# Kernel tuning notes

Hardware: AMD Instinct MI355X
Metric: run time of the kernel (lower is better)

## Reference

```python
import jax, jax.numpy as jnp
import numpy as np

EPS = 1e-5

def layernorm(x, g, b):
    mu = jnp.mean(x, axis=-1, keepdims=True)
    var = jnp.mean((x - mu) ** 2, axis=-1, keepdims=True)
    return (x - mu) * jax.lax.rsqrt(var + EPS) * g + b

def setup_inputs() -> dict:
    key = jax.random.key(0)
    B, T, C, H = 4, 2048, 1024, 16
    hs = C // H  # 64
    ks = jax.random.split(key, 16)
    s_in = 1.0 / np.sqrt(C)
    s_hid = 1.0 / np.sqrt(4 * C)
    return {
        "x":   jax.random.normal(ks[0], (B, T, C), jnp.float32),
        # per-head projections, stacked over heads: [H, C, hs]
        "Wq":  jax.random.normal(ks[1], (H, C, hs), jnp.float32) * s_in,
        "Wk":  jax.random.normal(ks[2], (H, C, hs), jnp.float32) * s_in,
        "Wv":  jax.random.normal(ks[3], (H, C, hs), jnp.float32) * s_in,
        # output projection [C, C] (concat of heads -> C)
        "Wo":  jax.random.normal(ks[4], (C, C), jnp.float32) * s_in,
        "bo":  jnp.zeros((C,), jnp.float32),
        # layernorm params
        "g1":  jnp.ones((C,), jnp.float32),
        "be1": jnp.zeros((C,), jnp.float32),
        "g2":  jnp.ones((C,), jnp.float32),
        "be2": jnp.zeros((C,), jnp.float32),
        # feed-forward: C -> 4C -> C
        "W1":  jax.random.normal(ks[5], (C, 4 * C), jnp.float32) * s_in,
        "b1":  jnp.zeros((4 * C,), jnp.float32),
        "W2":  jax.random.normal(ks[6], (4 * C, C), jnp.float32) * s_hid,
        "b2":  jnp.zeros((C,), jnp.float32),
    }

def reference(x, Wq, Wk, Wv, Wo, bo, g1, be1, g2, be2, W1, b1, W2, b2):
    B, T, C = x.shape
    H, _, hs = Wq.shape
    scale = hs ** -0.5

    # --- self-attention on ln1(x) ---
    xn = layernorm(x, g1, be1)
    q = jnp.einsum('btc,hcd->bhtd', xn, Wq)
    k = jnp.einsum('btc,hcd->bhtd', xn, Wk)
    v = jnp.einsum('btc,hcd->bhtd', xn, Wv)
    scores = jnp.einsum('bhtd,bhsd->bhts', q, k) * scale  # [B,H,T,T]
    causal = jnp.tril(jnp.ones((T, T), dtype=bool))
    scores = jnp.where(causal, scores, jnp.finfo(scores.dtype).min)
    wei = jax.nn.softmax(scores, axis=-1)
    out = jnp.einsum('bhts,bhsd->bhtd', wei, v)           # [B,H,T,hs]
    out = out.transpose(0, 2, 1, 3).reshape(B, T, H * hs)  # concat heads
    x = x + out @ Wo + bo

    # --- feed-forward on ln2(x) ---
    xn2 = layernorm(x, g2, be2)
    h = jax.nn.relu(xn2 @ W1 + b1)
    x = x + h @ W2 + b2
    return x
```

## Files before the change

### kernel.cpp

```cpp
#include <hip/hip_runtime.h>
#include <hip/hip_bf16.h>

typedef __hip_bfloat16 bf16;
typedef __attribute__((ext_vector_type(8))) short bf16x8;
typedef __attribute__((ext_vector_type(4))) short s16x4;
typedef __attribute__((ext_vector_type(4))) float f32x4;
typedef __attribute__((ext_vector_type(2))) unsigned int u32x2;

__device__ __forceinline__ float b2f(bf16 v) { return __bfloat162float(v); }
__device__ __forceinline__ bf16  f2b(float v) { return __float2bfloat16(v); }
__device__ __forceinline__ float ldf(const bf16* p)  { return __bfloat162float(*p); }
__device__ __forceinline__ float ldf(const float* p) { return *p; }
__device__ __forceinline__ void  stf(bf16* p, float v)  { *p = __float2bfloat16(v); }
__device__ __forceinline__ void  stf(float* p, float v) { *p = v; }

__device__ __forceinline__ unsigned cvt_pk_bf16(float lo, float hi) {
    unsigned r;
    asm("v_cvt_pk_bf16_f32 %0, %1, %2" : "=v"(r) : "v"(lo), "v"(hi));
    return r;
}

__device__ __forceinline__ void ld4(const float* p, float* v) {
    float4 t = *(const float4*)p;
    v[0] = t.x; v[1] = t.y; v[2] = t.z; v[3] = t.w;
}
__device__ __forceinline__ void ld4(const bf16* p, float* v) {
    s16x4 t = *(const s16x4*)p;
#pragma unroll
    for (int j = 0; j < 4; ++j) { short s = t[j]; v[j] = b2f(*(bf16*)&s); }
}

__device__ __forceinline__ void load_lds16(const bf16* g, short* lds) {
    __builtin_amdgcn_global_load_lds(
        (const __attribute__((address_space(1))) unsigned int*)g,
        (__attribute__((address_space(3))) unsigned int*)lds, 16, 0, 0);
}

template<typename InT>
__global__ __launch_bounds__(256) void ln_kernel(const InT* __restrict__ x,
                                                 const float* __restrict__ g,
                                                 const float* __restrict__ b,
                                                 bf16* __restrict__ out)
{
    const int C = 1024;
    int row = blockIdx.x;
    int tid = threadIdx.x;
    const InT* xr = x + (size_t)row * C;

    float v[4];
    ld4(xr + tid * 4, v);
    float s = 0.f, s2 = 0.f;
#pragma unroll
    for (int i = 0; i < 4; ++i) { s += v[i]; s2 += v[i] * v[i]; }
#pragma unroll
    for (int off = 32; off > 0; off >>= 1) {
        s  += __shfl_down(s,  off, 64);
        s2 += __shfl_down(s2, off, 64);
    }
    __shared__ float red[8];
    int wave = tid >> 6;
    if ((tid & 63) == 0) { red[wave] = s; red[wave + 4] = s2; }
    __syncthreads();
    float ts  = red[0] + red[1] + red[2] + red[3];
    float ts2 = red[4] + red[5] + red[6] + red[7];
    float mu  = ts * (1.f / 1024.f);
    float var = ts2 * (1.f / 1024.f) - mu * mu;
    float rstd = rsqrtf(var + 1e-5f);

    float4 gg = *(const float4*)(g + tid * 4);
    float4 bb = *(const float4*)(b + tid * 4);
    float gj[4] = {gg.x, gg.y, gg.z, gg.w};
    float bj[4] = {bb.x, bb.y, bb.z, bb.w};
    s16x4 o4;
#pragma unroll
    for (int j = 0; j < 4; ++j) {
        bf16 ob = f2b((v[j] - mu) * rstd * gj[j] + bj[j]);
        o4[j] = *(short*)&ob;
    }
    *(s16x4*)(out + (size_t)row * C + tid * 4) = o4;
}

__global__ __launch_bounds__(256) void prep_weights(
    const float* __restrict__ Wq, const float* __restrict__ Wk,
    const float* __restrict__ Wv, const float* __restrict__ Wo,
    const float* __restrict__ W1, const float* __restrict__ W2,
    bf16* __restrict__ wqkvt, bf16* __restrict__ wot,
    bf16* __restrict__ w1t, bf16* __restrict__ w2t)
{
    __shared__ float t[32][33];
    int tx = threadIdx.x & 31, ty = threadIdx.x >> 5;
    int id = blockIdx.x;
    const float* in; bf16* out; int in_ld, out_ld, n0, k0;
    if (id < 3072) {
        const float* Ws[3] = {Wq, Wk, Wv};
        int m = id >> 10, r = id & 1023;
        int z = r >> 6, rt = r & 63;
        in = Ws[m] + z * 65536;
        out = wqkvt + (size_t)(m * 1024 + z * 64) * 1024;
        in_ld = 64; out_ld = 1024;
        n0 = (rt & 1) * 32; k0 = (rt >> 1) * 32;
    } else if (id < 4096) {
        int r = id - 3072;
        in = Wo; out = wot; in_ld = 1024; out_ld = 1024;
        n0 = (r & 31) * 32; k0 = (r >> 5) * 32;
    } else if (id < 8192) {
        int r = id - 4096;
        in = W1; out = w1t; in_ld = 4096; out_ld = 1024;
        n0 = (r & 127) * 32; k0 = (r >> 7) * 32;
    } else {
        int r = id - 8192;
        in = W2; out = w2t; in_ld = 1024; out_ld = 4096;
        n0 = (r & 31) * 32; k0 = (r >> 5) * 32;
    }
#pragma unroll
    for (int i = 0; i < 4; ++i)
        t[ty + i * 8][tx] = in[(size_t)(k0 + ty + i * 8) * in_ld + n0 + tx];
    __syncthreads();
#pragma unroll
    for (int i = 0; i < 4; ++i)
        out[(size_t)(n0 + ty + i * 8) * out_ld + k0 + tx] = f2b(t[tx][ty + i * 8]);
}

__global__ __launch_bounds__(256) void vt_kernel(
    const bf16* __restrict__ qkv, bf16* __restrict__ vt, int T)
{
    __shared__ float t[32][33];
    int tx = threadIdx.x & 31, ty = threadIdx.x >> 5;
    int z = blockIdx.z, b = z >> 4, h = z & 15;
    const bf16* in = qkv + (size_t)b * T * 3072 + 2048 + h * 64;
    bf16* out = vt + (size_t)z * 64 * T;
    int n0 = blockIdx.x * 32, k0 = blockIdx.y * 32;
#pragma unroll
    for (int i = 0; i < 4; ++i)
        t[ty + i * 8][tx] = b2f(in[(size_t)(k0 + ty + i * 8) * 3072 + n0 + tx]);
    __syncthreads();
#pragma unroll
    for (int i = 0; i < 4; ++i)
        out[(size_t)(n0 + ty + i * 8) * T + k0 + tx] = f2b(t[tx][ty + i * 8]);
}

template<bool RELU, bool HAS_BIAS, typename OutT>
__global__ __launch_bounds__(512, 2) void gemm8p(
    const bf16* __restrict__ A, int lda,
    const bf16* __restrict__ Bt, int ldb,
    const float* __restrict__ bias,
    OutT* __restrict__ Cm, int ldc,
    int M, int N, int K)
{
    __shared__ short As[4][8192];
    __shared__ short Bs[4][8192];
    int tid = threadIdx.x, wv = tid >> 6, ln = tid & 63;
    int quad = ln >> 4, lane15 = ln & 15;

    int nbn = N >> 8;
    int nwg = gridDim.x;
    int f2 = (blockIdx.x & 7) * (nwg >> 3) + (blockIdx.x >> 3);
    int by = f2 / nbn, bx = f2 % nbn;
    int bm0 = by << 8, bn0 = bx << 8;

    int wr = wv >> 2, wc = wv & 3;
    const int NT = K >> 5;

    int sr = tid >> 2;
    int sc = ((tid & 3) ^ ((sr >> 1) & 3)) * 8;
    const bf16* Ab1 = A  + (size_t)(bm0 + sr) * lda + sc;
    const bf16* Ab2 = A  + (size_t)(bm0 + 128 + sr) * lda + sc;
    const bf16* Bb1 = Bt + (size_t)(bn0 + sr) * ldb + sc;
    const bf16* Bb2 = Bt + (size_t)(bn0 + 128 + sr) * ldb + sc;

#define STAGE_A8(bf_, u_) { \
    load_lds16(Ab1 + (u_) * 32, &As[bf_][wv * 512]); \
    load_lds16(Ab2 + (u_) * 32, &As[bf_][4096 + wv * 512]); }
#define STAGE_B8(bf_, u_) { \
    load_lds16(Bb1 + (u_) * 32, &Bs[bf_][wv * 512]); \
    load_lds16(Bb2 + (u_) * 32, &Bs[bf_][4096 + wv * 512]); }

    f32x4 acc[8][4] = {};
    int arow = wr * 128 + lane15;
    int brow = wc * 64 + lane15;
    int sw = (quad ^ ((lane15 >> 1) & 3)) * 8;

    STAGE_A8(0, 0); STAGE_B8(0, 0);
    STAGE_A8(1, 1); STAGE_B8(1, 1);
    STAGE_A8(2, 2); STAGE_B8(2, 2);
    asm volatile("s_waitcnt vmcnt(8)" ::: "memory");
    __builtin_amdgcn_s_barrier();

    for (int t = 0; t < NT; ++t) {
        int buf = t & 3;
        const short* Al = &As[buf][0];
        const short* Bl = &Bs[buf][0];

        bf16x8 af[4], bfr[4];
#pragma unroll
        for (int mi = 0; mi < 4; ++mi)
            af[mi] = *(const bf16x8*)&Al[(arow + mi * 16) * 32 + sw];
#pragma unroll
        for (int ni = 0; ni < 4; ++ni)
            bfr[ni] = *(const bf16x8*)&Bl[(brow + ni * 16) * 32 + sw];
        if (t + 3 < NT) STAGE_A8((t + 3) & 3, t + 3);
        __builtin_amdgcn_s_barrier();
        __builtin_amdgcn_s_setprio(1);
#pragma unroll
        for (int mi = 0; mi < 4; ++mi)
#pragma unroll
            for (int ni = 0; ni < 4; ++ni)
                acc[mi][ni] = __builtin_amdgcn_mfma_f32_16x16x32_bf16(
                    af[mi], bfr[ni], acc[mi][ni], 0, 0, 0);
        __builtin_amdgcn_s_setprio(0);
        __builtin_amdgcn_s_barrier();

        bf16x8 ag[4];
#pragma unroll
        for (int mi = 0; mi < 4; ++mi)
            ag[mi] = *(const bf16x8*)&Al[(arow + (mi + 4) * 16) * 32 + sw];
        if (t + 3 < NT) STAGE_B8((t + 3) & 3, t + 3);
        if (t < NT - 3) {
            asm volatile("s_waitcnt vmcnt(8)" ::: "memory");
        } else if (t == NT - 3) {
            asm volatile("s_waitcnt vmcnt(4)" ::: "memory");
        } else if (t == NT - 2) {
            asm volatile("s_waitcnt vmcnt(0)" ::: "memory");
        }
        __builtin_amdgcn_s_barrier();
        __builtin_amdgcn_s_setprio(1);
#pragma unroll
        for (int mi = 0; mi < 4; ++mi)
#pragma unroll
            for (int ni = 0; ni < 4; ++ni)
                acc[mi + 4][ni] = __builtin_amdgcn_mfma_f32_16x16x32_bf16(
                    ag[mi], bfr[ni], acc[mi + 4][ni], 0, 0, 0);
        __builtin_amdgcn_s_setprio(0);
        __builtin_amdgcn_s_barrier();
    }

#undef STAGE_A8
#undef STAGE_B8

#pragma unroll
    for (int mi = 0; mi < 8; ++mi) {
#pragma unroll
        for (int r = 0; r < 4; ++r) {
            int gm = bm0 + wr * 128 + mi * 16 + quad * 4 + r;
#pragma unroll
            for (int ni = 0; ni < 4; ++ni) {
                int gn = bn0 + wc * 64 + ni * 16 + lane15;
                float v = acc[mi][ni][r];
                if (HAS_BIAS) v += bias[gn];
                if (RELU)     v = fmaxf(v, 0.f);
                stf(Cm + (size_t)gm * ldc + gn, v);
            }
        }
    }
}

template<int BK, bool RELU, bool HAS_BIAS, bool HAS_RES, typename ResT, typename OutT>
__global__ __launch_bounds__(256) void gemm_bt(
    const bf16* __restrict__ A, int lda,
    const bf16* __restrict__ Bt, int ldb,
    const float* __restrict__ bias,
    const ResT* __restrict__ res, int ldr,
    OutT* __restrict__ Cm, int ldc,
    int M, int N, int K)
{
    __shared__ short As[2][128 * BK];
    __shared__ short Bs[2][128 * BK];
    int tid = threadIdx.x, wv = tid >> 6, ln = tid & 63;

    int f = blockIdx.x + blockIdx.y * gridDim.x;
    int nby = gridDim.y;
    int by = f % nby, bx = f / nby;
    int bm0 = by * 128, bn0 = bx * 128;

    int wm = (wv & 1) * 64, wn = (wv >> 1) * 64;
    int quad = ln >> 4, lane15 = ln & 15;

    f32x4 acc[4][4] = {};

    const bf16* Ab = A + (size_t)bm0 * lda;
    const bf16* Bb = Bt + (size_t)bn0 * ldb;

    auto stage = [&](int buf, int kk) {
        if constexpr (BK == 32) {
            int srow = ln >> 2;
            int scol = (((ln & 3) ^ ((ln >> 3) & 3)) * 8);
#pragma unroll
            for (int i = 0; i < 2; ++i) {
                int ch = wv + i * 4;
                load_lds16(Ab + (size_t)(ch * 16 + srow) * lda + kk + scol,
                           &As[buf][ch * 16 * 32]);
                load_lds16(Bb + (size_t)(ch * 16 + srow) * ldb + kk + scol,
                           &Bs[buf][ch * 16 * 32]);
            }
        } else {
            int srow = ln >> 3;
            int scol = ((ln & 7) ^ srow) * 8;
#pragma unroll
            for (int i = 0; i < 4; ++i) {
                int r0 = i * 32 + wv * 8;
                load_lds16(Ab + (size_t)(r0 + srow) * lda + kk + scol,
                           &As[buf][r0 * 64]);
                load_lds16(Bb + (size_t)(r0 + srow) * ldb + kk + scol,
                           &Bs[buf][r0 * 64]);
            }
        }
    };

    stage(0, 0);
    __syncthreads();

    int cur = 0;
    for (int k0 = 0; k0 < K; k0 += BK) {
        if (k0 + BK < K) stage(cur ^ 1, k0 + BK);
        if constexpr (BK == 32) {
            int sw = (quad ^ ((lane15 >> 1) & 3)) * 8;
            bf16x8 af[4], bfr[4];
#pragma unroll
            for (int mi = 0; mi < 4; ++mi)
                af[mi] = *(const bf16x8*)&As[cur][(wm + mi * 16 + lane15) * 32 + sw];
#pragma unroll
            for (int ni = 0; ni < 4; ++ni)
                bfr[ni] = *(const bf16x8*)&Bs[cur][(wn + ni * 16 + lane15) * 32 + sw];
#pragma unroll
            for (int mi = 0; mi < 4; ++mi)
#pragma unroll
                for (int ni = 0; ni < 4; ++ni)
                    acc[mi][ni] = __builtin_amdgcn_mfma_f32_16x16x32_bf16(
                        af[mi], bfr[ni], acc[mi][ni], 0, 0, 0);
        } else {
#pragma unroll
            for (int ks = 0; ks < 2; ++ks) {
                int sw = (((ks * 4 + quad) ^ (lane15 & 7)) * 8);
                bf16x8 af[4], bfr[4];
#pragma unroll
                for (int mi = 0; mi < 4; ++mi)
                    af[mi] = *(const bf16x8*)&As[cur][(wm + mi * 16 + lane15) * 64 + sw];
#pragma unroll
                for (int ni = 0; ni < 4; ++ni)
                    bfr[ni] = *(const bf16x8*)&Bs[cur][(wn + ni * 16 + lane15) * 64 + sw];
#pragma unroll
                for (int mi = 0; mi < 4; ++mi)
#pragma unroll
                    for (int ni = 0; ni < 4; ++ni)
                        acc[mi][ni] = __builtin_amdgcn_mfma_f32_16x16x32_bf16(
                            af[mi], bfr[ni], acc[mi][ni], 0, 0, 0);
            }
        }
        __syncthreads();
        cur ^= 1;
    }

#pragma unroll
    for (int mi = 0; mi < 4; ++mi) {
#pragma unroll
        for (int r = 0; r < 4; ++r) {
            int gm = bm0 + wm + mi * 16 + quad * 4 + r;
#pragma unroll
            for (int ni = 0; ni < 4; ++ni) {
                int gn = bn0 + wn + ni * 16 + lane15;
                float v = acc[mi][ni][r];
                if (HAS_BIAS) v += bias[gn];
                if (HAS_RES)  v += ldf(res + (size_t)gm * ldr + gn);
                if (RELU)     v = fmaxf(v, 0.f);
                stf(Cm + (size_t)gm * ldc + gn, v);
            }
        }
    }
}

__device__ __forceinline__ void attn_tile_q(
    const short* __restrict__ Ks, const short* __restrict__ Vs,
    short* __restrict__ Psw,
    const bf16x8* qf, f32x4* oacc, float& lrun,
    int ktbase, int qmin, int quad, int lane15, int r7)
{
    const float scale2 = 0.18033688011112042f;
    const int PS = 72;
    f32x4 sacc[4] = {};
    __builtin_amdgcn_s_setprio(1);
#pragma unroll
    for (int ks = 0; ks < 2; ++ks) {
        int so = ((ks * 4 + quad) ^ r7) * 8;
#pragma unroll
        for (int mi = 0; mi < 4; ++mi) {
            bf16x8 kf = *(const bf16x8*)&Ks[(mi * 16 + lane15) * 64 + so];
            sacc[mi] = __builtin_amdgcn_mfma_f32_16x16x32_bf16(kf, qf[ks], sacc[mi], 0, 0, 0);
        }
    }
    __builtin_amdgcn_s_setprio(0);

    if (ktbase + 63 > qmin) {
        int ql = qmin + lane15;
#pragma unroll
        for (int mi = 0; mi < 4; ++mi)
#pragma unroll
            for (int r = 0; r < 4; ++r)
                if (ktbase + mi * 16 + quad * 4 + r > ql) sacc[mi][r] = -3e38f;
    }

    float psum = 0.f;
#pragma unroll
    for (int mi = 0; mi < 4; ++mi) {
        float p[4];
#pragma unroll
        for (int r = 0; r < 4; ++r) {
            p[r] = exp2f(sacc[mi][r] * scale2);
            psum += p[r];
        }
        u32x2 pu;
        pu[0] = cvt_pk_bf16(p[0], p[1]);
        pu[1] = cvt_pk_bf16(p[2], p[3]);
        *(u32x2*)&Psw[lane15 * PS + mi * 16 + quad * 4] = pu;
    }
    lrun += psum;

    __builtin_amdgcn_s_setprio(1);
#pragma unroll
    for (int ks = 0; ks < 2; ++ks) {
        int so = ((ks * 4 + quad) ^ r7) * 8;
        bf16x8 pf = *(const bf16x8*)&Psw[lane15 * PS + ks * 32 + quad * 8];
#pragma unroll
        for (int di = 0; di < 4; ++di) {
            bf16x8 vf = *(const bf16x8*)&Vs[(di * 16 + lane15) * 64 + so];
            oacc[di] = __builtin_amdgcn_mfma_f32_16x16x32_bf16(vf, pf, oacc[di], 0, 0, 0);
        }
    }
    __builtin_amdgcn_s_setprio(0);
}

__global__ __launch_bounds__(512, 4) void attn_kernel(
    const bf16* __restrict__ qkv, const bf16* __restrict__ vt,
    bf16* __restrict__ o, int T)
{
    const int LDQ = 3072;
    const int PS = 72;
    int bx = blockIdx.x;
    int qta = 15 - bx;
    int qtb = bx;
    int h = blockIdx.y, b = blockIdx.z;
    int tid = threadIdx.x, wv = tid >> 6, ln = tid & 63;
    int quad = ln >> 4, lane15 = ln & 15, r7 = lane15 & 7;

    __shared__ short KV[2][2][64 * 64];
    __shared__ short Ps[2][8][16 * PS];

    int lr = ln >> 3;
    int lc = ((ln & 7) ^ lr) * 8;

    const bf16* kbase = qkv + (size_t)(b * T) * LDQ + 1024 + h * 64;
    const bf16* vbase = vt + (size_t)((b * 16 + h) * 64) * T;

#pragma unroll
    for (int i = 0; i < 2; ++i) {
        int ch = wv * 2 + i;
        load_lds16(qkv + (size_t)(b * T + qta * 128 + ch * 8 + lr) * LDQ + h * 64 + lc,
                   &KV[0][0][ch * 512]);
        load_lds16(qkv + (size_t)(b * T + qtb * 128 + ch * 8 + lr) * LDQ + h * 64 + lc,
                   &KV[1][0][ch * 512]);
    }
    __syncthreads();
    bf16x8 qfa[2], qfb[2];
#pragma unroll
    for (int ks = 0; ks < 2; ++ks) {
        int off = (wv * 16 + lane15) * 64 + (((ks * 4 + quad) ^ r7) * 8);
        qfa[ks] = *(const bf16x8*)&KV[0][0][off];
        qfb[ks] = *(const bf16x8*)&KV[1][0][off];
    }
    __syncthreads();

    f32x4 oacca[4] = {}, oaccb[4] = {};
    float lra = 0.f, lrb = 0.f;
    int qmina = qta * 128 + wv * 16;
    int qminb = qtb * 128 + wv * 16;
    int ntiles = 2 * qta + 2;

    const bf16* kp = kbase + (size_t)(wv * 8 + lr) * LDQ + lc;
    const bf16* vp = vbase + (size_t)(wv * 8 + lr) * T + lc;
    load_lds16(kp, &KV[0][0][wv * 8 * 64]);
    load_lds16(vp, &KV[0][1][wv * 8 * 64]);

    for (int kt = 0; kt < ntiles; ++kt) {
        __syncthreads();
        if (kt + 1 < ntiles) {
            int nb = (kt + 1) & 1;
            kp += 64 * LDQ;
            vp += 64;
            load_lds16(kp, &KV[nb][0][wv * 8 * 64]);
            load_lds16(vp, &KV[nb][1][wv * 8 * 64]);
        }
        const short* Ks = &KV[kt & 1][0][0];
        const short* Vs = &KV[kt & 1][1][0];
        int kb = kt * 64;

        if (kb <= qmina + 15)
            attn_tile_q(Ks, Vs, &Ps[0][wv][0], qfa, oacca, lra,
                        kb, qmina, quad, lane15, r7);
        if (kb <= qminb + 15)
            attn_tile_q(Ks, Vs, &Ps[1][wv][0], qfb, oaccb, lrb,
                        kb, qminb, quad, lane15, r7);
    }

    lra += __shfl_xor(lra, 16, 64);
    lra += __shfl_xor(lra, 32, 64);
    float inva = 1.f / lra;
    size_t rowa = (size_t)(b * T + qta * 128 + wv * 16 + lane15);
#pragma unroll
    for (int di = 0; di < 4; ++di) {
        u32x2 ou;
        ou[0] = cvt_pk_bf16(oacca[di][0] * inva, oacca[di][1] * inva);
        ou[1] = cvt_pk_bf16(oacca[di][2] * inva, oacca[di][3] * inva);
        *(u32x2*)&o[rowa * 1024 + h * 64 + di * 16 + quad * 4] = ou;
    }

    lrb += __shfl_xor(lrb, 16, 64);
    lrb += __shfl_xor(lrb, 32, 64);
    float invb = 1.f / lrb;
    size_t rowb = (size_t)(b * T + qtb * 128 + wv * 16 + lane15);
#pragma unroll
    for (int di = 0; di < 4; ++di) {
        u32x2 ou;
        ou[0] = cvt_pk_bf16(oaccb[di][0] * invb, oaccb[di][1] * invb);
        ou[1] = cvt_pk_bf16(oaccb[di][2] * invb, oaccb[di][3] * invb);
        *(u32x2*)&o[rowb * 1024 + h * 64 + di * 16 + quad * 4] = ou;
    }
}

extern "C" void kernel_launch(void* const* d_in, const int* in_sizes, int n_in,
                              void* d_out, int out_size, void* d_ws, size_t ws_size,
                              hipStream_t stream)
{
    (void)in_sizes; (void)n_in; (void)out_size; (void)ws_size;
    const float* x   = (const float*)d_in[0];
    const float* Wq  = (const float*)d_in[1];
    const float* Wk  = (const float*)d_in[2];
    const float* Wv  = (const float*)d_in[3];
    const float* Wo  = (const float*)d_in[4];
    const float* bo  = (const float*)d_in[5];
    const float* g1  = (const float*)d_in[6];
    const float* be1 = (const float*)d_in[7];
    const float* g2  = (const float*)d_in[8];
    const float* be2 = (const float*)d_in[9];
    const float* W1  = (const float*)d_in[10];
    const float* b1  = (const float*)d_in[11];
    const float* W2  = (const float*)d_in[12];
    const float* b2  = (const float*)d_in[13];

    const int T = 2048, M = 4 * T;
    const size_t MB = 1ull << 20;
    char* ws = (char*)d_ws;

    bf16*  xn    = (bf16*)(ws + 0 * MB);
    bf16*  qkv   = (bf16*)(ws + 16 * MB);
    bf16*  vt    = (bf16*)(ws + 64 * MB);
    bf16*  wqkvt = (bf16*)(ws + 80 * MB);
    bf16*  x1b   = (bf16*)(ws + 80 * MB);
    bf16*  wot   = (bf16*)(ws + 96 * MB);
    bf16*  xn2   = (bf16*)(ws + 96 * MB);
    bf16*  w1t   = (bf16*)(ws + 112 * MB);
    bf16*  w2t   = (bf16*)(ws + 120 * MB);
    bf16*  attnb = (bf16*)(ws + 0 * MB);
    bf16*  hb    = (bf16*)(ws + 0 * MB);

    dim3 blk(256);

    prep_weights<<<12288, blk, 0, stream>>>(Wq, Wk, Wv, Wo, W1, W2,
                                            wqkvt, wot, w1t, w2t);

    ln_kernel<float><<<M, blk, 0, stream>>>(x, g1, be1, xn);

    gemm8p<false, false, bf16><<<dim3(384), dim3(512), 0, stream>>>(
        xn, 1024, wqkvt, 1024, nullptr, qkv, 3072, M, 3072, 1024);

    vt_kernel<<<dim3(2, T / 32, 64), blk, 0, stream>>>(qkv, vt, T);

    attn_kernel<<<dim3(8, 16, 4), dim3(512), 0, stream>>>(qkv, vt, attnb, T);

    gemm_bt<32, false, true, true, float, bf16><<<dim3(8, 64), blk, 0, stream>>>(
        attnb, 1024, wot, 1024, bo, x, 1024, x1b, 1024, M, 1024, 1024);

    ln_kernel<bf16><<<M, blk, 0, stream>>>(x1b, g2, be2, xn2);

    gemm8p<true, true, bf16><<<dim3(512), dim3(512), 0, stream>>>(
        xn2, 1024, w1t, 1024, b1, hb, 4096, M, 4096, 1024);

    gemm_bt<64, false, true, true, bf16, float><<<dim3(8, 64), blk, 0, stream>>>(
        hb, 4096, w2t, 4096, b2, x1b, 1024, (float*)d_out, 1024, M, 1024, 4096);
}
```

Measured before the change: 486.8 us.

## Switch attention to 32x32 MFMA tiles with register-resident softmax probabilities

Rewrites the attention inner tile to use 32x32x16 bf16 MFMAs with 256-row query tiles per block, so each wave handles 32 queries. The softmax probabilities stay in registers and are reshuffled with permlane32_swap instead of being staged through LDS. The dual-query path now shares each K/V fragment load across both query tiles. Q fragments are loaded directly from global memory rather than via LDS. The trade-off is higher register pressure: launch bounds drop to 2 blocks per SM and the grid is halved, which reduces occupancy and parallelism.

```diff
diff --git a/kernel.cpp b/kernel.cpp
--- a/kernel.cpp
+++ b/kernel.cpp
@@ -5,7 +5,9 @@
 typedef __attribute__((ext_vector_type(8))) short bf16x8;
 typedef __attribute__((ext_vector_type(4))) short s16x4;
 typedef __attribute__((ext_vector_type(4))) float f32x4;
+typedef __attribute__((ext_vector_type(16))) float f32x16;
 typedef __attribute__((ext_vector_type(2))) unsigned int u32x2;
+typedef __attribute__((ext_vector_type(4))) unsigned int u32x4;
 
 __device__ __forceinline__ float b2f(bf16 v) { return __bfloat162float(v); }
 __device__ __forceinline__ bf16  f2b(float v) { return __float2bfloat16(v); }
@@ -368,81 +370,106 @@
     }
 }
 
-__device__ __forceinline__ void attn_tile_q(
+template<bool DUAL>
+__device__ __forceinline__ void attn_tile32(
     const short* __restrict__ Ks, const short* __restrict__ Vs,
-    short* __restrict__ Psw,
-    const bf16x8* qf, f32x4* oacc, float& lrun,
-    int ktbase, int qmin, int quad, int lane15, int r7)
+    const bf16x8* qfa, const bf16x8* qfb,
+    f32x16* oa, f32x16* ob, float& lra, float& lrb,
+    int kb, int qmina, int qminb, int l31, int hi, int l7)
 {
     const float scale2 = 0.18033688011112042f;
-    const int PS = 72;
-    f32x4 sacc[4] = {};
+    f32x16 sa[2] = {};
+    f32x16 sb[2] = {};
+
     __builtin_amdgcn_s_setprio(1);
 #pragma unroll
-    for (int ks = 0; ks < 2; ++ks) {
-        int so = ((ks * 4 + quad) ^ r7) * 8;
-#pragma unroll
-        for (int mi = 0; mi < 4; ++mi) {
-            bf16x8 kf = *(const bf16x8*)&Ks[(mi * 16 + lane15) * 64 + so];
-            sacc[mi] = __builtin_amdgcn_mfma_f32_16x16x32_bf16(kf, qf[ks], sacc[mi], 0, 0, 0);
+    for (int ts = 0; ts < 2; ++ts) {
+#pragma unroll
+        for (int ks = 0; ks < 4; ++ks) {
+            bf16x8 kf = *(const bf16x8*)&Ks[(ts * 32 + l31) * 64 + (((ks * 2 + hi) ^ l7) * 8)];
+            sa[ts] = __builtin_amdgcn_mfma_f32_32x32x16_bf16(kf, qfa[ks], sa[ts], 0, 0, 0);
+            if (DUAL)
+                sb[ts] = __builtin_amdgcn_mfma_f32_32x32x16_bf16(kf, qfb[ks], sb[ts], 0, 0, 0);
         }
     }
     __builtin_amdgcn_s_setprio(0);
 
-    if (ktbase + 63 > qmin) {
-        int ql = qmin + lane15;
-#pragma unroll
-        for (int mi = 0; mi < 4; ++mi)
-#pragma unroll
-            for (int r = 0; r < 4; ++r)
-                if (ktbase + mi * 16 + quad * 4 + r > ql) sacc[mi][r] = -3e38f;
-    }
-
-    float psum = 0.f;
-#pragma unroll
-    for (int mi = 0; mi < 4; ++mi) {
-        float p[4];
-#pragma unroll
-        for (int r = 0; r < 4; ++r) {
-            p[r] = exp2f(sacc[mi][r] * scale2);
-            psum += p[r];
-        }
-        u32x2 pu;
-        pu[0] = cvt_pk_bf16(p[0], p[1]);
-        pu[1] = cvt_pk_bf16(p[2], p[3]);
-        *(u32x2*)&Psw[lane15 * PS + mi * 16 + quad * 4] = pu;
-    }
-    lrun += psum;
+    int qmin = DUAL ? qminb : qmina;
+    if (kb + 63 > qmin) {
+        int qcap = qmin + l31;
+#pragma unroll
+        for (int ts = 0; ts < 2; ++ts)
+#pragma unroll
+            for (int r = 0; r < 16; ++r) {
+                int key = kb + ts * 32 + (r & 3) + 8 * (r >> 2) + 4 * hi;
+                if (key > qcap) {
+                    if (DUAL) sb[ts][r] = -3e38f; else sa[ts][r] = -3e38f;
+                }
+            }
+    }
+
+    float psa = 0.f, psb = 0.f;
+#pragma unroll
+    for (int ts = 0; ts < 2; ++ts)
+#pragma unroll
+        for (int r = 0; r < 16; ++r) {
+            float va = exp2f(sa[ts][r] * scale2);
+            sa[ts][r] = va; psa += va;
+            if (DUAL) {
+                float vb = exp2f(sb[ts][r] * scale2);
+                sb[ts][r] = vb; psb += vb;
+            }
+        }
+    lra += psa;
+    if (DUAL) lrb += psb;
 
     __builtin_amdgcn_s_setprio(1);
 #pragma unroll
-    for (int ks = 0; ks < 2; ++ks) {
-        int so = ((ks * 4 + quad) ^ r7) * 8;
-        bf16x8 pf = *(const bf16x8*)&Psw[lane15 * PS + ks * 32 + quad * 8];
-#pragma unroll
-        for (int di = 0; di < 4; ++di) {
-            bf16x8 vf = *(const bf16x8*)&Vs[(di * 16 + lane15) * 64 + so];
-            oacc[di] = __builtin_amdgcn_mfma_f32_16x16x32_bf16(vf, pf, oacc[di], 0, 0, 0);
+    for (int s = 0; s < 4; ++s) {
+        const int ts = s >> 1, q0 = (s & 1) * 8;
+        unsigned a0 = cvt_pk_bf16(sa[ts][q0 + 0], sa[ts][q0 + 1]);
+        unsigned a1 = cvt_pk_bf16(sa[ts][q0 + 2], sa[ts][q0 + 3]);
+        unsigned a2 = cvt_pk_bf16(sa[ts][q0 + 4], sa[ts][q0 + 5]);
+        unsigned a3 = cvt_pk_bf16(sa[ts][q0 + 6], sa[ts][q0 + 7]);
+        u32x2 s02 = __builtin_amdgcn_permlane32_swap(a0, a2, false, false);
+        u32x2 s13 = __builtin_amdgcn_permlane32_swap(a1, a3, false, false);
+        u32x4 fa = {s02[0], s13[0], s02[1], s13[1]};
+        bf16x8 pfa = *(bf16x8*)&fa;
+        bf16x8 pfb;
+        if (DUAL) {
+            unsigned b0 = cvt_pk_bf16(sb[ts][q0 + 0], sb[ts][q0 + 1]);
+            unsigned b1 = cvt_pk_bf16(sb[ts][q0 + 2], sb[ts][q0 + 3]);
+            unsigned b2 = cvt_pk_bf16(sb[ts][q0 + 4], sb[ts][q0 + 5]);
+            unsigned b3 = cvt_pk_bf16(sb[ts][q0 + 6], sb[ts][q0 + 7]);
+            u32x2 t02 = __builtin_amdgcn_permlane32_swap(b0, b2, false, false);
+            u32x2 t13 = __builtin_amdgcn_permlane32_swap(b1, b3, false, false);
+            u32x4 fb = {t02[0], t13[0], t02[1], t13[1]};
+            pfb = *(bf16x8*)&fb;
+        }
+#pragma unroll
+        for (int dt = 0; dt < 2; ++dt) {
+            bf16x8 vf = *(const bf16x8*)&Vs[(dt * 32 + l31) * 64 + (((s * 2 + hi) ^ l7) * 8)];
+            oa[dt] = __builtin_amdgcn_mfma_f32_32x32x16_bf16(vf, pfa, oa[dt], 0, 0, 0);
+            if (DUAL)
+                ob[dt] = __builtin_amdgcn_mfma_f32_32x32x16_bf16(vf, pfb, ob[dt], 0, 0, 0);
         }
     }
     __builtin_amdgcn_s_setprio(0);
 }
 
-__global__ __launch_bounds__(512, 4) void attn_kernel(
+__global__ __launch_bounds__(512, 2) void attn_kernel(
     const bf16* __restrict__ qkv, const bf16* __restrict__ vt,
     bf16* __restrict__ o, int T)
 {
     const int LDQ = 3072;
-    const int PS = 72;
     int bx = blockIdx.x;
-    int qta = 15 - bx;
+    int qta = 7 - bx;
     int qtb = bx;
     int h = blockIdx.y, b = blockIdx.z;
     int tid = threadIdx.x, wv = tid >> 6, ln = tid & 63;
-    int quad = ln >> 4, lane15 = ln & 15, r7 = lane15 & 7;
+    int l31 = ln & 31, hi = ln >> 5, l7 = ln & 7;
 
     __shared__ short KV[2][2][64 * 64];
-    __shared__ short Ps[2][8][16 * PS];
 
     int lr = ln >> 3;
     int lc = ((ln & 7) ^ lr) * 8;
@@ -450,29 +477,22 @@
     const bf16* kbase = qkv + (size_t)(b * T) * LDQ + 1024 + h * 64;
     const bf16* vbase = vt + (size_t)((b * 16 + h) * 64) * T;
 
-#pragma unroll
-    for (int i = 0; i < 2; ++i) {
-        int ch = wv * 2 + i;
-        load_lds16(qkv + (size_t)(b * T + qta * 128 + ch * 8 + lr) * LDQ + h * 64 + lc,
-                   &KV[0][0][ch * 512]);
-        load_lds16(qkv + (size_t)(b * T + qtb * 128 + ch * 8 + lr) * LDQ + h * 64 + lc,
-                   &KV[1][0][ch * 512]);
-    }
-    __syncthreads();
-    bf16x8 qfa[2], qfb[2];
-#pragma unroll
-    for (int ks = 0; ks < 2; ++ks) {
-        int off = (wv * 16 + lane15) * 64 + (((ks * 4 + quad) ^ r7) * 8);
-        qfa[ks] = *(const bf16x8*)&KV[0][0][off];
-        qfb[ks] = *(const bf16x8*)&KV[1][0][off];
-    }
-    __syncthreads();
-
-    f32x4 oacca[4] = {}, oaccb[4] = {};
+    bf16x8 qfa[4], qfb[4];
+    {
+        const bf16* qa = qkv + (size_t)(b * T + qta * 256 + wv * 32 + l31) * LDQ + h * 64 + hi * 8;
+        const bf16* qb = qkv + (size_t)(b * T + qtb * 256 + wv * 32 + l31) * LDQ + h * 64 + hi * 8;
+#pragma unroll
+        for (int ks = 0; ks < 4; ++ks) {
+            qfa[ks] = *(const bf16x8*)(qa + ks * 16);
+            qfb[ks] = *(const bf16x8*)(qb + ks * 16);
+        }
+    }
+
+    f32x16 oa[2] = {}, ob[2] = {};
     float lra = 0.f, lrb = 0.f;
-    int qmina = qta * 128 + wv * 16;
-    int qminb = qtb * 128 + wv * 16;
-    int ntiles = 2 * qta + 2;
+    int qmina = qta * 256 + wv * 32;
+    int qminb = qtb * 256 + wv * 32;
+    int ntiles = (qta + 1) * 4;
 
     const bf16* kp = kbase + (size_t)(wv * 8 + lr) * LDQ + lc;
     const bf16* vp = vbase + (size_t)(wv * 8 + lr) * T + lc;
@@ -492,37 +512,39 @@
         const short* Vs = &KV[kt & 1][1][0];
         int kb = kt * 64;
 
-        if (kb <= qmina + 15)
-            attn_tile_q(Ks, Vs, &Ps[0][wv][0], qfa, oacca, lra,
-                        kb, qmina, quad, lane15, r7);
-        if (kb <= qminb + 15)
-            attn_tile_q(Ks, Vs, &Ps[1][wv][0], qfb, oaccb, lrb,
-                        kb, qminb, quad, lane15, r7);
-    }
-
-    lra += __shfl_xor(lra, 16, 64);
+        if (kb <= qminb + 31)
+            attn_tile32<true>(Ks, Vs, qfa, qfb, oa, ob, lra, lrb,
+                              kb, qmina, qminb, l31, hi, l7);
+        else if (kb <= qmina + 31)
+            attn_tile32<false>(Ks, Vs, qfa, qfb, oa, ob, lra, lrb,
+                               kb, qmina, qminb, l31, hi, l7);
+    }
+
     lra += __shfl_xor(lra, 32, 64);
     float inva = 1.f / lra;
-    size_t rowa = (size_t)(b * T + qta * 128 + wv * 16 + lane15);
-#pragma unroll
-    for (int di = 0; di < 4; ++di) {
-        u32x2 ou;
-        ou[0] = cvt_pk_bf16(oacca[di][0] * inva, oacca[di][1] * inva);
-        ou[1] = cvt_pk_bf16(oacca[di][2] * inva, oacca[di][3] * inva);
-        *(u32x2*)&o[rowa * 1024 + h * 64 + di * 16 + quad * 4] = ou;
-    }
-
-    lrb += __shfl_xor(lrb, 16, 64);
+    size_t rowa = (size_t)(b * T + qta * 256 + wv * 32 + l31);
+#pragma unroll
+    for (int dt = 0; dt < 2; ++dt)
+#pragma unroll
+        for (int rq = 0; rq < 4; ++rq) {
+            u32x2 ou;
+            ou[0] = cvt_pk_bf16(oa[dt][rq * 4 + 0] * inva, oa[dt][rq * 4 + 1] * inva);
+            ou[1] = cvt_pk_bf16(oa[dt][rq * 4 + 2] * inva, oa[dt][rq * 4 + 3] * inva);
+            *(u32x2*)&o[rowa * 1024 + h * 64 + dt * 32 + rq * 8 + hi * 4] = ou;
+        }
+
     lrb += __shfl_xor(lrb, 32, 64);
     float invb = 1.f / lrb;
-    size_t rowb = (size_t)(b * T + qtb * 128 + wv * 16 + lane15);
-#pragma unroll
-    for (int di = 0; di < 4; ++di) {
-        u32x2 ou;
-        ou[0] = cvt_pk_bf16(oaccb[di][0] * invb, oaccb[di][1] * invb);
-        ou[1] = cvt_pk_bf16(oaccb[di][2] * invb, oaccb[di][3] * invb);
-        *(u32x2*)&o[rowb * 1024 + h * 64 + di * 16 + quad * 4] = ou;
-    }
+    size_t rowb = (size_t)(b * T + qtb * 256 + wv * 32 + l31);
+#pragma unroll
+    for (int dt = 0; dt < 2; ++dt)
+#pragma unroll
+        for (int rq = 0; rq < 4; ++rq) {
+            u32x2 ou;
+            ou[0] = cvt_pk_bf16(ob[dt][rq * 4 + 0] * invb, ob[dt][rq * 4 + 1] * invb);
+            ou[1] = cvt_pk_bf16(ob[dt][rq * 4 + 2] * invb, ob[dt][rq * 4 + 3] * invb);
+            *(u32x2*)&o[rowb * 1024 + h * 64 + dt * 32 + rq * 8 + hi * 4] = ou;
+        }
 }
 
 extern "C" void kernel_launch(void* const* d_in, const int* in_sizes, int n_in,
@@ -573,7 +595,7 @@
 
     vt_kernel<<<dim3(2, T / 32, 64), blk, 0, stream>>>(qkv, vt, T);
 
-    attn_kernel<<<dim3(8, 16, 4), dim3(512), 0, stream>>>(qkv, vt, attnb, T);
+    attn_kernel<<<dim3(4, 16, 4), dim3(512), 0, stream>>>(qkv, vt, attnb, T);
 
     gemm_bt<32, false, true, true, float, bf16><<<dim3(8, 64), blk, 0, stream>>>(
         attnb, 1024, wot, 1024, bo, x, 1024, x1b, 1024, M, 1024, 1024);
```

Result: no change. 485.8 us (-0.2%).
